# Performance work log

Hardware: AMD Instinct MI355X
Metric: run time of the kernel (lower is better)

The kernel has to match this reference:

```python
import jax, jax.numpy as jnp
import numpy as np

B, L, D, DQK = 4, 4096, 2048, 2048
THRESH = 0.5
N_TARGET = 6.0
RATIO_W = 0.03
EPS = 1e-8  # torch cosine_similarity eps


def setup_inputs() -> dict:
    key = jax.random.key(0)
    k1, k2, k3 = jax.random.split(key, 3)
    tokens = jax.random.normal(k1, (B, L, D), jnp.float32)
    W_qk = jax.random.normal(k2, (D, 2 * DQK), jnp.float32) * 0.02
    start_key = jax.random.normal(k3, (DQK,), jnp.float32) * 0.01
    return {"tokens": tokens, "W_qk": W_qk, "start_key": start_key}


def _cosine_sim(a, b):
    na = jnp.maximum(jnp.linalg.norm(a, axis=-1), EPS)
    nb = jnp.maximum(jnp.linalg.norm(b, axis=-1), EPS)
    return jnp.sum(a * b, axis=-1) / (na * nb)


def _gated_scan(gates, x):
    # h_t = gates_t * h_{t-1} + x_t, along axis 1 (first-order linear recurrence)
    def combine(c1, c2):
        a1, b1 = c1
        a2, b2 = c2
        return a1 * a2, a2 * b1 + b2
    g = gates[..., None]  # [B, L, 1] broadcasts against x [B, L, D]
    _, h = jax.lax.associative_scan(combine, (g, x), axis=1)
    return h


def _forward(tokens, W_qk, start_key, needs_grad):
    qk = tokens @ W_qk                                  # [B, L, 2*DQK]
    queries, keys = jnp.split(qk, 2, axis=-1)
    start = jnp.broadcast_to(start_key, (tokens.shape[0], 1, start_key.shape[-1]))
    keys_shifted = jnp.concatenate([start, keys[:, :-1]], axis=1)  # keys[:, :-1] after prepend
    cos = _cosine_sim(queries, keys_shifted)            # [B, L]
    probs = (1.0 - cos) * 0.5
    boundary = (probs > THRESH).at[:, 0].set(True)      # [B, L] bool

    # Jagged pack: compact boundary positions to the front of each row (stable order),
    # padded to full length L with zeros (torch pads to max num_chunks; same values).
    order = jnp.argsort(~boundary, axis=-1, stable=True)            # [B, L]
    valid = jnp.take_along_axis(boundary, order, axis=-1)           # first num_chunks True
    down = jnp.take_along_axis(tokens, order[..., None], axis=1)    # [B, L, D]
    down = jnp.where(valid[..., None], down, 0.0)
    bprobs = jnp.where(valid, jnp.take_along_axis(probs, order, axis=-1), 0.0)

    gates = 1.0 - bprobs
    down = down * bprobs[..., None]
    smoothed = _gated_scan(gates, down)                 # [B, L, D] (padded downsampled)

    # Upsample: each position t reads the chunk of its most recent boundary
    # (equivalent to repeat_interleave over chunk_lens in the torch code).
    chunk_id = jnp.cumsum(boundary.astype(jnp.int32), axis=-1) - 1  # [B, L]
    upsampled = jnp.take_along_axis(smoothed, chunk_id[..., None], axis=1)

    if needs_grad:
        confidence = jnp.where(boundary, probs, 1.0 - probs)
        scale = confidence * jax.lax.stop_gradient(1.0 - confidence)
        upsampled = upsampled * scale[..., None]
        F = jnp.mean(boundary.astype(probs.dtype), axis=-1)
        G = jnp.mean(probs, axis=-1)
        aux = N_TARGET / (N_TARGET - 1.0) * ((N_TARGET - 1.0) * F * G + (1.0 - F) * (1.0 - G))
        aux_loss = jnp.mean(aux) * RATIO_W
    else:
        aux_loss = jnp.zeros((), probs.dtype)
    return smoothed, upsampled, aux_loss


def reference(tokens, W_qk, start_key):
    # Inference path (tokens.requires_grad == False in torch): no output scale, zero aux loss.
    return _forward(tokens, W_qk, start_key, needs_grad=False)
```

## Files before the change

### kernel.cpp

```cpp
#include <hip/hip_runtime.h>
#include <math.h>

#define Bq_ 4
#define Lq_ 4096
#define Dq_ 2048
#define Mq_ 16384
#define NW_ 4096
#define DQK_ 2048
#define NSLOT 32
#define BM_ 256
#define BN_ 128
#define NSEG 16
#define SEGLEN 256
#define BUFSZ 66560
#define BOFF_ 33792

typedef short s8v __attribute__((ext_vector_type(8)));
typedef float f4v __attribute__((ext_vector_type(4)));

#define GLDS16(g, l) __builtin_amdgcn_global_load_lds( \
    (const __attribute__((address_space(1))) unsigned int*)(g), \
    (__attribute__((address_space(3))) unsigned int*)(l), 16, 0, 0)

__device__ __forceinline__ void bf16split(float x, unsigned short& h, unsigned short& l) {
    unsigned u = __float_as_uint(x);
    unsigned hb = (u + 0x7FFFu + ((u >> 16) & 1u)) & 0xFFFF0000u;
    float fh = __uint_as_float(hb);
    float r = x - fh;
    unsigned ur = __float_as_uint(r);
    unsigned lb = (ur + 0x7FFFu + ((ur >> 16) & 1u)) >> 16;
    h = (unsigned short)(hb >> 16);
    l = (unsigned short)lb;
}

__global__ __launch_bounds__(256) void split_kernel(const float* __restrict__ in,
                                                    unsigned short* __restrict__ hi,
                                                    unsigned short* __restrict__ lo,
                                                    int n4) {
    int stride = gridDim.x * 256;
    for (int i = blockIdx.x * 256 + threadIdx.x; i < n4; i += stride) {
        float4 v = ((const float4*)in)[i];
        float vv[4] = {v.x, v.y, v.z, v.w};
        unsigned short hh[4], ll[4];
#pragma unroll
        for (int j = 0; j < 4; ++j) bf16split(vv[j], hh[j], ll[j]);
        ushort4 h4 = make_ushort4(hh[0], hh[1], hh[2], hh[3]);
        ushort4 l4 = make_ushort4(ll[0], ll[1], ll[2], ll[3]);
        ((ushort4*)hi)[i] = h4;
        ((ushort4*)lo)[i] = l4;
    }
}

__global__ __launch_bounds__(256) void wsplitT_kernel(const float* __restrict__ W,
                                                      unsigned short* __restrict__ hiT,
                                                      unsigned short* __restrict__ loT) {
    __shared__ float tile[64][65];
    int k0 = blockIdx.x * 64, n0 = blockIdx.y * 64;
    int tid = threadIdx.x;
#pragma unroll
    for (int e = 0; e < 16; ++e) {
        int idx = e * 256 + tid;
        int r = idx >> 6, j = idx & 63;
        tile[r][j] = W[(size_t)(k0 + r) * NW_ + n0 + j];
    }
    __syncthreads();
#pragma unroll
    for (int e = 0; e < 16; ++e) {
        int idx = e * 256 + tid;
        int nn = idx >> 6, kk = idx & 63;
        unsigned short h, l;
        bf16split(tile[kk][nn], h, l);
        size_t o = (size_t)(n0 + nn) * DQK_ + k0 + kk;
        hiT[o] = h;
        loT[o] = l;
    }
}

__global__ __launch_bounds__(256) void wqs_kernel(const float* __restrict__ W,
                                                  const float* __restrict__ s,
                                                  float* __restrict__ w) {
    int d = blockIdx.x;
    int tid = threadIdx.x;
    float acc = 0.f;
    const float* row = W + (size_t)d * NW_;
    for (int j = tid; j < DQK_; j += 256) acc += row[j] * s[j];
    __shared__ float red[256];
    red[tid] = acc;
    __syncthreads();
    for (int off = 128; off > 0; off >>= 1) {
        if (tid < off) red[tid] += red[tid + off];
        __syncthreads();
    }
    if (tid == 0) w[d] = red[0];
}

__global__ __launch_bounds__(256) void l0_kernel(const float* __restrict__ tokens,
                                                 const float* __restrict__ s,
                                                 const float* __restrict__ w,
                                                 float* __restrict__ c0,
                                                 float* __restrict__ snorm) {
    int b = blockIdx.x;
    int tid = threadIdx.x;
    float acc = 0.f;
    if (b < Bq_) {
        const float* t = tokens + (size_t)b * Lq_ * Dq_;
        for (int dd = tid; dd < Dq_; dd += 256) acc += t[dd] * w[dd];
    } else {
        for (int jj = tid; jj < DQK_; jj += 256) acc += s[jj] * s[jj];
    }
    __shared__ float red[256];
    red[tid] = acc;
    __syncthreads();
    for (int off = 128; off > 0; off >>= 1) {
        if (tid < off) red[tid] += red[tid + off];
        __syncthreads();
    }
    if (tid == 0) {
        if (b < Bq_) c0[b] = red[0];
        else snorm[0] = red[0];
    }
}

__global__ __launch_bounds__(512, 2) void gemm_kernel(const unsigned short* __restrict__ Thi,
                                                      const unsigned short* __restrict__ Tlo,
                                                      const unsigned short* __restrict__ Whi,
                                                      const unsigned short* __restrict__ Wlo,
                                                      float* __restrict__ pa,
                                                      float* __restrict__ pkn,
                                                      float* __restrict__ pcn) {
    extern __shared__ char smc[];

    int id = blockIdx.x;
    int nt = id & 15;
    int mt = id >> 4;
    int r0 = mt * BM_;
    int c0 = nt * BN_;
    int tid = threadIdx.x;
    int lane = tid & 63, w = tid >> 6;
    int wm = w >> 1, wn = w & 1;
    int lr = lane & 15, lg = lane >> 4;

    int rl = tid >> 3;
    int ch = tid & 7;
    int s = ch ^ (rl & 7);
    const unsigned short* aptr = (s < 4) ? Thi : Tlo;
    const unsigned short* bptr = (s < 4) ? Whi : Wlo;
    int ako = (s & 3) * 8;
    int aoff[4], boff[4];
#pragma unroll
    for (int i = 0; i < 4; ++i) {
        int g = r0 - 1 + i * 64 + rl;
        g = g < 0 ? 0 : (g > Mq_ - 1 ? Mq_ - 1 : g);
        aoff[i] = g * Dq_ + ako;
    }
#pragma unroll
    for (int i = 0; i < 4; ++i) {
        int j = i * 64 + rl;
        int wr = j < 128 ? c0 + j : DQK_ + c0 + (j - 128);
        boff[i] = wr * DQK_ + ako;
    }
    int rlX = 256 + (lane >> 3);
    int sX = (lane & 7) ^ ((lane >> 3) & 7);
    const unsigned short* aptrX = (sX < 4) ? Thi : Tlo;
    int gX = r0 - 1 + rlX;
    gX = gX > Mq_ - 1 ? Mq_ - 1 : gX;
    int aoffX = gX * Dq_ + (sX & 3) * 8;

    int aq_ad[4], ak_ad[4], bq_ad[4], bk_ad[4];
#pragma unroll
    for (int rf = 0; rf < 4; ++rf) {
        int rq = wm * 64 + rf * 16 + lr + 1;
        int rk = rq - 1;
        aq_ad[rf] = rq * 128 + ((lg ^ (rq & 7)) * 16);
        ak_ad[rf] = rk * 128 + ((lg ^ (rk & 7)) * 16);
    }
#pragma unroll
    for (int cf = 0; cf < 4; ++cf) {
        int rbq = wn * 64 + cf * 16 + lr;
        int rbk = rbq + 128;
        bq_ad[cf] = rbq * 128 + ((lg ^ (rbq & 7)) * 16);
        bk_ad[cf] = rbk * 128 + ((lg ^ (rbk & 7)) * 16);
    }

    f4v accq[4][4], acck[4][4];
#pragma unroll
    for (int rf = 0; rf < 4; ++rf)
#pragma unroll
        for (int cf = 0; cf < 4; ++cf) {
            accq[rf][cf] = (f4v){0.f, 0.f, 0.f, 0.f};
            acck[rf][cf] = (f4v){0.f, 0.f, 0.f, 0.f};
        }

#define STAGE(buf, k0e)                                                     \
    {                                                                       \
        char* bA = smc + (buf) * BUFSZ;                                     \
        char* bB = bA + BOFF_;                                              \
        _Pragma("unroll")                                                   \
        for (int i = 0; i < 4; ++i)                                         \
            GLDS16(aptr + aoff[i] + (k0e), bA + (i * 64 + w * 8) * 128);    \
        if (w == 0)                                                         \
            GLDS16(aptrX + aoffX + (k0e), bA + 256 * 128);                  \
        _Pragma("unroll")                                                   \
        for (int i = 0; i < 4; ++i)                                         \
            GLDS16(bptr + boff[i] + (k0e), bB + (i * 64 + w * 8) * 128);    \
    }

    int cur = 0;
    STAGE(0, 0);
    __syncthreads();

    for (int kt = 0; kt < 64; ++kt) {
        if (kt < 63) STAGE(cur ^ 1, (kt + 1) * 32);

        const char* bA = smc + cur * BUFSZ;
        const char* bB = bA + BOFF_;
        s8v aqh[4], aql[4], akh[4], akl[4];
#pragma unroll
        for (int rf = 0; rf < 4; ++rf) {
            aqh[rf] = *(const s8v*)(bA + aq_ad[rf]);
            aql[rf] = *(const s8v*)(bA + (aq_ad[rf] ^ 64));
            akh[rf] = *(const s8v*)(bA + ak_ad[rf]);
            akl[rf] = *(const s8v*)(bA + (ak_ad[rf] ^ 64));
        }
#pragma unroll
        for (int cf = 0; cf < 4; ++cf) {
            s8v bqh = *(const s8v*)(bB + bq_ad[cf]);
            s8v bql = *(const s8v*)(bB + (bq_ad[cf] ^ 64));
            s8v bkh = *(const s8v*)(bB + bk_ad[cf]);
            s8v bkl = *(const s8v*)(bB + (bk_ad[cf] ^ 64));
#pragma unroll
            for (int rf = 0; rf < 4; ++rf) {
                accq[rf][cf] = __builtin_amdgcn_mfma_f32_16x16x32_bf16(aqh[rf], bqh, accq[rf][cf], 0, 0, 0);
                accq[rf][cf] = __builtin_amdgcn_mfma_f32_16x16x32_bf16(aqh[rf], bql, accq[rf][cf], 0, 0, 0);
                accq[rf][cf] = __builtin_amdgcn_mfma_f32_16x16x32_bf16(aql[rf], bqh, accq[rf][cf], 0, 0, 0);
                acck[rf][cf] = __builtin_amdgcn_mfma_f32_16x16x32_bf16(akh[rf], bkh, acck[rf][cf], 0, 0, 0);
                acck[rf][cf] = __builtin_amdgcn_mfma_f32_16x16x32_bf16(akh[rf], bkl, acck[rf][cf], 0, 0, 0);
                acck[rf][cf] = __builtin_amdgcn_mfma_f32_16x16x32_bf16(akl[rf], bkh, acck[rf][cf], 0, 0, 0);
            }
        }
        __syncthreads();
        cur ^= 1;
    }
#undef STAGE

    size_t o = (size_t)(nt * 2 + wn) * Mq_;
#pragma unroll
    for (int rf = 0; rf < 4; ++rf) {
        int rbase = r0 + wm * 64 + rf * 16 + lg * 4;
#pragma unroll
        for (int jj = 0; jj < 4; ++jj) {
            float sq = 0.f, sk = 0.f, sc = 0.f;
#pragma unroll
            for (int cf = 0; cf < 4; ++cf) {
                float q = accq[rf][cf][jj];
                float k = acck[rf][cf][jj];
                sq = fmaf(q, q, sq);
                sk = fmaf(k, k, sk);
                sc = fmaf(q, k, sc);
            }
#pragma unroll
            for (int m = 1; m < 16; m <<= 1) {
                sq += __shfl_xor(sq, m);
                sk += __shfl_xor(sk, m);
                sc += __shfl_xor(sc, m);
            }
            if (lr == 0) {
                int r = rbase + jj;
                pa[o + r] = sq;
                pcn[o + r] = sc;
                pkn[o + r] = sk;
            }
        }
    }
}

__global__ __launch_bounds__(256) void rowstat_kernel(const float* __restrict__ pa,
                                                      const float* __restrict__ pkn,
                                                      const float* __restrict__ pcn,
                                                      const float* __restrict__ c0,
                                                      const float* __restrict__ snorm,
                                                      float* __restrict__ probs) {
    int r = blockIdx.x * 256 + threadIdx.x;
    float a = 0.f, bb = 0.f, c = 0.f;
    for (int s = 0; s < NSLOT; ++s) {
        size_t o = (size_t)s * Mq_;
        a += pa[o + r];
        c += pcn[o + r];
        bb += pkn[o + r];
    }
    if ((r & (Lq_ - 1)) == 0) { c = c0[r >> 12]; bb = snorm[0]; }
    float na = fmaxf(sqrtf(a), 1e-8f);
    float nb = fmaxf(sqrtf(bb), 1e-8f);
    float cosv = c / (na * nb);
    probs[r] = (1.f - cosv) * 0.5f;
}

__global__ __launch_bounds__(256) void pack_kernel(const float* __restrict__ probs,
                                                   int* __restrict__ posArr,
                                                   float* __restrict__ pprob,
                                                   int* __restrict__ cid,
                                                   int* __restrict__ nch,
                                                   float* __restrict__ aux) {
    int b = blockIdx.x;
    int tid = threadIdx.x;
    int base = b * Lq_ + tid * 16;
#pragma unroll
    for (int u = 0; u < 16; ++u) {
        posArr[base + u] = 0;
        pprob[base + u] = 0.f;
    }
    float p[16];
    bool bd[16];
    int c = 0;
#pragma unroll
    for (int u = 0; u < 16; ++u) {
        p[u] = probs[base + u];
        bd[u] = (p[u] > 0.5f) || (tid == 0 && u == 0);
        c += bd[u] ? 1 : 0;
    }
    __shared__ int sc[256];
    sc[tid] = c;
    __syncthreads();
    for (int off = 1; off < 256; off <<= 1) {
        int t = (tid >= off) ? sc[tid - off] : 0;
        __syncthreads();
        sc[tid] += t;
        __syncthreads();
    }
    int idx = sc[tid] - c;
#pragma unroll
    for (int u = 0; u < 16; ++u) {
        if (bd[u]) {
            posArr[b * Lq_ + idx] = tid * 16 + u;
            pprob[b * Lq_ + idx] = p[u];
            idx++;
        }
        cid[base + u] = idx - 1;
    }
    if (tid == 255) nch[b] = sc[255];
    if (b == 0 && tid == 0) aux[0] = 0.0f;
}

__global__ __launch_bounds__(256) void segend_kernel(const float* __restrict__ tokens,
                                                     const int* __restrict__ posArr,
                                                     const float* __restrict__ pprob,
                                                     float* __restrict__ hseg,
                                                     float* __restrict__ segGate) {
    int b = blockIdx.z, s = blockIdx.y;
    int ch = blockIdx.x * 256 + threadIdx.x;
    const float* tb = tokens + (size_t)b * Lq_ * Dq_ + ch;
    const int* pos = posArr + b * Lq_ + s * SEGLEN;
    const float* pp = pprob + b * Lq_ + s * SEGLEN;
    float h = 0.f;
    for (int u = 0; u < SEGLEN; ++u) {
        float pv = pp[u];
        int t0 = pos[u];
        h = fmaf(1.f - pv, h, tb[(size_t)t0 * Dq_] * pv);
    }
    hseg[((size_t)b * NSEG + s) * Dq_ + ch] = h;
    __shared__ float g_[256];
    if (blockIdx.x == 0) {
        g_[threadIdx.x] = 1.f - pp[threadIdx.x];
        __syncthreads();
        if (threadIdx.x == 0) {
            float P = 1.f;
            for (int i = 0; i < 256; ++i) P *= g_[i];
            segGate[b * NSEG + s] = P;
        }
    }
}

__global__ __launch_bounds__(256) void carry_kernel(const float* __restrict__ hseg,
                                                    const float* __restrict__ segGate,
                                                    float* __restrict__ carryArr) {
    int idx = blockIdx.x * 256 + threadIdx.x;
    int b = idx >> 11;
    int ch = idx & 2047;
    float carry = 0.f;
#pragma unroll
    for (int s = 0; s < NSEG; ++s) {
        size_t o = ((size_t)b * NSEG + s) * Dq_ + ch;
        carryArr[o] = carry;
        carry = hseg[o] + carry * segGate[b * NSEG + s];
    }
}

__global__ __launch_bounds__(256) void scan3_kernel(const float* __restrict__ tokens,
                                                    const int* __restrict__ posArr,
                                                    const float* __restrict__ pprob,
                                                    const float* __restrict__ carryArr,
                                                    float* __restrict__ out_sm) {
    int b = blockIdx.z, s = blockIdx.y;
    int ch = blockIdx.x * 256 + threadIdx.x;
    const float* tb = tokens + (size_t)b * Lq_ * Dq_ + ch;
    const int* pos = posArr + b * Lq_ + s * SEGLEN;
    const float* pp = pprob + b * Lq_ + s * SEGLEN;
    float* sm = out_sm + (size_t)b * Lq_ * Dq_ + (size_t)s * SEGLEN * Dq_ + ch;
    float h = carryArr[((size_t)b * NSEG + s) * Dq_ + ch];
    for (int u = 0; u < SEGLEN; ++u) {
        float pv = pp[u];
        int t0 = pos[u];
        h = fmaf(1.f - pv, h, tb[(size_t)t0 * Dq_] * pv);
        sm[(size_t)u * Dq_] = h;
    }
}

__global__ __launch_bounds__(256) void upsample_kernel(const float* __restrict__ sm,
                                                       const int* __restrict__ cid,
                                                       float* __restrict__ up) {
    int r = blockIdx.x;
    int b = r >> 12;
    int c = cid[r];
    const float* src = sm + ((size_t)b * Lq_ + c) * Dq_;
    float* dst = up + (size_t)r * Dq_;
    int tid = threadIdx.x;
    *(float4*)&dst[tid * 8] = *(const float4*)&src[tid * 8];
    *(float4*)&dst[tid * 8 + 4] = *(const float4*)&src[tid * 8 + 4];
}

extern "C" void kernel_launch(void* const* d_in, const int* in_sizes, int n_in,
                              void* d_out, int out_size, void* d_ws, size_t ws_size,
                              hipStream_t stream) {
    const float* tokens = (const float*)d_in[0];
    const float* W = (const float*)d_in[1];
    const float* s = (const float*)d_in[2];

    float* out = (float*)d_out;
    float* out_sm = out;
    float* out_up = out + (size_t)Mq_ * Dq_;
    float* out_aux = out + 2 * (size_t)Mq_ * Dq_;

    unsigned short* Thi = (unsigned short*)out_up;
    unsigned short* Tlo = (unsigned short*)((char*)out_up + 67108864);
    unsigned short* WhiT = (unsigned short*)out_sm;
    unsigned short* WloT = (unsigned short*)((char*)out_sm + 16777216);

    float* ws = (float*)d_ws;
    float* pa = ws;
    float* pkn = pa + (size_t)NSLOT * Mq_;
    float* pcn = pkn + (size_t)NSLOT * Mq_;
    float* probs = pcn + (size_t)NSLOT * Mq_;
    float* w = probs + Mq_;
    float* c0 = w + DQK_;
    float* snorm = c0 + 4;
    float* pprob = snorm + 4;
    int* posArr = (int*)(pprob + Mq_);
    int* cid = posArr + Mq_;
    int* nch = cid + Mq_;
    float* hseg = (float*)(nch + 8);
    float* segGate = hseg + Bq_ * NSEG * Dq_;
    float* carryArr = segGate + 64;

    split_kernel<<<2048, 256, 0, stream>>>(tokens, Thi, Tlo, Mq_ * Dq_ / 4);
    wsplitT_kernel<<<dim3(32, 64), 256, 0, stream>>>(W, WhiT, WloT);
    wqs_kernel<<<DQK_, 256, 0, stream>>>(W, s, w);
    l0_kernel<<<Bq_ + 1, 256, 0, stream>>>(tokens, s, w, c0, snorm);

    hipFuncSetAttribute(reinterpret_cast<const void*>(gemm_kernel),
                        hipFuncAttributeMaxDynamicSharedMemorySize, 2 * BUFSZ);
    gemm_kernel<<<1024, 512, 2 * BUFSZ, stream>>>(Thi, Tlo, WhiT, WloT, pa, pkn, pcn);

    rowstat_kernel<<<Mq_ / 256, 256, 0, stream>>>(pa, pkn, pcn, c0, snorm, probs);
    pack_kernel<<<Bq_, 256, 0, stream>>>(probs, posArr, pprob, cid, nch, out_aux);
    segend_kernel<<<dim3(8, NSEG, Bq_), 256, 0, stream>>>(tokens, posArr, pprob, hseg, segGate);
    carry_kernel<<<32, 256, 0, stream>>>(hseg, segGate, carryArr);
    scan3_kernel<<<dim3(8, NSEG, Bq_), 256, 0, stream>>>(tokens, posArr, pprob, carryArr, out_sm);
    upsample_kernel<<<Mq_, 256, 0, stream>>>(out_sm, cid, out_up);
}
```

Measured before the change: 750.5 us.

## Use 32x32 MFMA tiles in GEMM and fuse upsample into scan kernel

The GEMM inner loop moves from 16x16x32 bf16 MFMA fragments to 32x32x16 fragments, with the LDS addressing and the epilogue row-reduction remapped to the 32x32 output layout. This aims for higher MFMA throughput and fewer LDS fragment reads per FLOP. Separately, the upsample kernel is removed: scan3 now writes each smoothed chunk value directly to every upsampled position in that chunk's range. That avoids re-reading the smoothed output, but it creates load imbalance when chunk lengths vary, since long chunks mean long serial write loops in some segments.

```diff
diff --git a/kernel.cpp b/kernel.cpp
--- a/kernel.cpp
+++ b/kernel.cpp
@@ -16,7 +16,7 @@
 #define BOFF_ 33792
 
 typedef short s8v __attribute__((ext_vector_type(8)));
-typedef float f4v __attribute__((ext_vector_type(4)));
+typedef float f16v __attribute__((ext_vector_type(16)));
 
 #define GLDS16(g, l) __builtin_amdgcn_global_load_lds( \
     (const __attribute__((address_space(1))) unsigned int*)(g), \
@@ -138,7 +138,7 @@
     int tid = threadIdx.x;
     int lane = tid & 63, w = tid >> 6;
     int wm = w >> 1, wn = w & 1;
-    int lr = lane & 15, lg = lane >> 4;
+    int hh = lane >> 5, l5 = lane & 31;
 
     int rl = tid >> 3;
     int ch = tid & 7;
@@ -166,29 +166,38 @@
     gX = gX > Mq_ - 1 ? Mq_ - 1 : gX;
     int aoffX = gX * Dq_ + (sX & 3) * 8;
 
-    int aq_ad[4], ak_ad[4], bq_ad[4], bk_ad[4];
-#pragma unroll
-    for (int rf = 0; rf < 4; ++rf) {
-        int rq = wm * 64 + rf * 16 + lr + 1;
-        int rk = rq - 1;
-        aq_ad[rf] = rq * 128 + ((lg ^ (rq & 7)) * 16);
-        ak_ad[rf] = rk * 128 + ((lg ^ (rk & 7)) * 16);
-    }
-#pragma unroll
-    for (int cf = 0; cf < 4; ++cf) {
-        int rbq = wn * 64 + cf * 16 + lr;
-        int rbk = rbq + 128;
-        bq_ad[cf] = rbq * 128 + ((lg ^ (rbq & 7)) * 16);
-        bk_ad[cf] = rbk * 128 + ((lg ^ (rbk & 7)) * 16);
-    }
-
-    f4v accq[4][4], acck[4][4];
-#pragma unroll
-    for (int rf = 0; rf < 4; ++rf)
-#pragma unroll
-        for (int cf = 0; cf < 4; ++cf) {
-            accq[rf][cf] = (f4v){0.f, 0.f, 0.f, 0.f};
-            acck[rf][cf] = (f4v){0.f, 0.f, 0.f, 0.f};
+    int aq_ad[2][2], ak_ad[2][2], bq_ad[2][2], bk_ad[2][2];
+#pragma unroll
+    for (int mf = 0; mf < 2; ++mf)
+#pragma unroll
+        for (int ks = 0; ks < 2; ++ks) {
+            int rq = wm * 64 + mf * 32 + l5 + 1;
+            int rk = rq - 1;
+            int c = ks * 2 + hh;
+            aq_ad[mf][ks] = rq * 128 + ((c ^ (rq & 7)) * 16);
+            ak_ad[mf][ks] = rk * 128 + ((c ^ (rk & 7)) * 16);
+        }
+#pragma unroll
+    for (int nf = 0; nf < 2; ++nf)
+#pragma unroll
+        for (int ks = 0; ks < 2; ++ks) {
+            int rbq = wn * 64 + nf * 32 + l5;
+            int rbk = rbq + 128;
+            int c = ks * 2 + hh;
+            bq_ad[nf][ks] = rbq * 128 + ((c ^ (rbq & 7)) * 16);
+            bk_ad[nf][ks] = rbk * 128 + ((c ^ (rbk & 7)) * 16);
+        }
+
+    f16v accq[2][2], acck[2][2];
+#pragma unroll
+    for (int mf = 0; mf < 2; ++mf)
+#pragma unroll
+        for (int nf = 0; nf < 2; ++nf) {
+#pragma unroll
+            for (int e = 0; e < 16; ++e) {
+                accq[mf][nf][e] = 0.f;
+                acck[mf][nf][e] = 0.f;
+            }
         }
 
 #define STAGE(buf, k0e)                                                     \
@@ -214,28 +223,31 @@
 
         const char* bA = smc + cur * BUFSZ;
         const char* bB = bA + BOFF_;
-        s8v aqh[4], aql[4], akh[4], akl[4];
-#pragma unroll
-        for (int rf = 0; rf < 4; ++rf) {
-            aqh[rf] = *(const s8v*)(bA + aq_ad[rf]);
-            aql[rf] = *(const s8v*)(bA + (aq_ad[rf] ^ 64));
-            akh[rf] = *(const s8v*)(bA + ak_ad[rf]);
-            akl[rf] = *(const s8v*)(bA + (ak_ad[rf] ^ 64));
-        }
-#pragma unroll
-        for (int cf = 0; cf < 4; ++cf) {
-            s8v bqh = *(const s8v*)(bB + bq_ad[cf]);
-            s8v bql = *(const s8v*)(bB + (bq_ad[cf] ^ 64));
-            s8v bkh = *(const s8v*)(bB + bk_ad[cf]);
-            s8v bkl = *(const s8v*)(bB + (bk_ad[cf] ^ 64));
-#pragma unroll
-            for (int rf = 0; rf < 4; ++rf) {
-                accq[rf][cf] = __builtin_amdgcn_mfma_f32_16x16x32_bf16(aqh[rf], bqh, accq[rf][cf], 0, 0, 0);
-                accq[rf][cf] = __builtin_amdgcn_mfma_f32_16x16x32_bf16(aqh[rf], bql, accq[rf][cf], 0, 0, 0);
-                accq[rf][cf] = __builtin_amdgcn_mfma_f32_16x16x32_bf16(aql[rf], bqh, accq[rf][cf], 0, 0, 0);
-                acck[rf][cf] = __builtin_amdgcn_mfma_f32_16x16x32_bf16(akh[rf], bkh, acck[rf][cf], 0, 0, 0);
-                acck[rf][cf] = __builtin_amdgcn_mfma_f32_16x16x32_bf16(akh[rf], bkl, acck[rf][cf], 0, 0, 0);
-                acck[rf][cf] = __builtin_amdgcn_mfma_f32_16x16x32_bf16(akl[rf], bkh, acck[rf][cf], 0, 0, 0);
+#pragma unroll
+        for (int ks = 0; ks < 2; ++ks) {
+            s8v aqh[2], aql[2], akh[2], akl[2];
+#pragma unroll
+            for (int mf = 0; mf < 2; ++mf) {
+                aqh[mf] = *(const s8v*)(bA + aq_ad[mf][ks]);
+                aql[mf] = *(const s8v*)(bA + (aq_ad[mf][ks] ^ 64));
+                akh[mf] = *(const s8v*)(bA + ak_ad[mf][ks]);
+                akl[mf] = *(const s8v*)(bA + (ak_ad[mf][ks] ^ 64));
+            }
+#pragma unroll
+            for (int nf = 0; nf < 2; ++nf) {
+                s8v bqh = *(const s8v*)(bB + bq_ad[nf][ks]);
+                s8v bql = *(const s8v*)(bB + (bq_ad[nf][ks] ^ 64));
+                s8v bkh = *(const s8v*)(bB + bk_ad[nf][ks]);
+                s8v bkl = *(const s8v*)(bB + (bk_ad[nf][ks] ^ 64));
+#pragma unroll
+                for (int mf = 0; mf < 2; ++mf) {
+                    accq[mf][nf] = __builtin_amdgcn_mfma_f32_32x32x16_bf16(aqh[mf], bqh, accq[mf][nf], 0, 0, 0);
+                    accq[mf][nf] = __builtin_amdgcn_mfma_f32_32x32x16_bf16(aqh[mf], bql, accq[mf][nf], 0, 0, 0);
+                    accq[mf][nf] = __builtin_amdgcn_mfma_f32_32x32x16_bf16(aql[mf], bqh, accq[mf][nf], 0, 0, 0);
+                    acck[mf][nf] = __builtin_amdgcn_mfma_f32_32x32x16_bf16(akh[mf], bkh, acck[mf][nf], 0, 0, 0);
+                    acck[mf][nf] = __builtin_amdgcn_mfma_f32_32x32x16_bf16(akh[mf], bkl, acck[mf][nf], 0, 0, 0);
+                    acck[mf][nf] = __builtin_amdgcn_mfma_f32_32x32x16_bf16(akl[mf], bkh, acck[mf][nf], 0, 0, 0);
+                }
             }
         }
         __syncthreads();
@@ -245,27 +257,27 @@
 
     size_t o = (size_t)(nt * 2 + wn) * Mq_;
 #pragma unroll
-    for (int rf = 0; rf < 4; ++rf) {
-        int rbase = r0 + wm * 64 + rf * 16 + lg * 4;
-#pragma unroll
-        for (int jj = 0; jj < 4; ++jj) {
+    for (int mf = 0; mf < 2; ++mf) {
+        int rb0 = r0 + wm * 64 + mf * 32 + hh * 4;
+#pragma unroll
+        for (int reg = 0; reg < 16; ++reg) {
             float sq = 0.f, sk = 0.f, sc = 0.f;
 #pragma unroll
-            for (int cf = 0; cf < 4; ++cf) {
-                float q = accq[rf][cf][jj];
-                float k = acck[rf][cf][jj];
+            for (int nf = 0; nf < 2; ++nf) {
+                float q = accq[mf][nf][reg];
+                float k = acck[mf][nf][reg];
                 sq = fmaf(q, q, sq);
                 sk = fmaf(k, k, sk);
                 sc = fmaf(q, k, sc);
             }
 #pragma unroll
-            for (int m = 1; m < 16; m <<= 1) {
+            for (int m = 1; m < 32; m <<= 1) {
                 sq += __shfl_xor(sq, m);
                 sk += __shfl_xor(sk, m);
                 sc += __shfl_xor(sc, m);
             }
-            if (lr == 0) {
-                int r = rbase + jj;
+            if (l5 == 0) {
+                int r = rb0 + (reg & 3) + 8 * (reg >> 2);
                 pa[o + r] = sq;
                 pcn[o + r] = sc;
                 pkn[o + r] = sk;
@@ -389,33 +401,30 @@
                                                     const int* __restrict__ posArr,
                                                     const float* __restrict__ pprob,
                                                     const float* __restrict__ carryArr,
-                                                    float* __restrict__ out_sm) {
+                                                    const int* __restrict__ nch,
+                                                    float* __restrict__ out_sm,
+                                                    float* __restrict__ out_up) {
     int b = blockIdx.z, s = blockIdx.y;
     int ch = blockIdx.x * 256 + threadIdx.x;
+    int nc = nch[b];
     const float* tb = tokens + (size_t)b * Lq_ * Dq_ + ch;
     const int* pos = posArr + b * Lq_ + s * SEGLEN;
     const float* pp = pprob + b * Lq_ + s * SEGLEN;
     float* sm = out_sm + (size_t)b * Lq_ * Dq_ + (size_t)s * SEGLEN * Dq_ + ch;
+    float* upb = out_up + (size_t)b * Lq_ * Dq_ + ch;
     float h = carryArr[((size_t)b * NSEG + s) * Dq_ + ch];
     for (int u = 0; u < SEGLEN; ++u) {
+        int c = s * SEGLEN + u;
         float pv = pp[u];
         int t0 = pos[u];
         h = fmaf(1.f - pv, h, tb[(size_t)t0 * Dq_] * pv);
         sm[(size_t)u * Dq_] = h;
-    }
-}
-
-__global__ __launch_bounds__(256) void upsample_kernel(const float* __restrict__ sm,
-                                                       const int* __restrict__ cid,
-                                                       float* __restrict__ up) {
-    int r = blockIdx.x;
-    int b = r >> 12;
-    int c = cid[r];
-    const float* src = sm + ((size_t)b * Lq_ + c) * Dq_;
-    float* dst = up + (size_t)r * Dq_;
-    int tid = threadIdx.x;
-    *(float4*)&dst[tid * 8] = *(const float4*)&src[tid * 8];
-    *(float4*)&dst[tid * 8 + 4] = *(const float4*)&src[tid * 8 + 4];
+        if (c < nc) {
+            int tend = (c + 1 < nc) ? posArr[b * Lq_ + c + 1] : Lq_;
+            for (int t = t0; t < tend; ++t)
+                upb[(size_t)t * Dq_] = h;
+        }
+    }
 }
 
 extern "C" void kernel_launch(void* const* d_in, const int* in_sizes, int n_in,
@@ -464,6 +473,5 @@
     pack_kernel<<<Bq_, 256, 0, stream>>>(probs, posArr, pprob, cid, nch, out_aux);
     segend_kernel<<<dim3(8, NSEG, Bq_), 256, 0, stream>>>(tokens, posArr, pprob, hseg, segGate);
     carry_kernel<<<32, 256, 0, stream>>>(hseg, segGate, carryArr);
-    scan3_kernel<<<dim3(8, NSEG, Bq_), 256, 0, stream>>>(tokens, posArr, pprob, carryArr, out_sm);
-    upsample_kernel<<<Mq_, 256, 0, stream>>>(out_sm, cid, out_up);
-}
+    scan3_kernel<<<dim3(8, NSEG, Bq_), 256, 0, stream>>>(tokens, posArr, pprob, carryArr, nch, out_sm, out_up);
+}
```

Result: slower. 1.013 ms (+34.9%).
